# Kernel optimization log

Hardware: AMD Instinct MI355X
Metric: run time of the kernel (lower is better)

## Reference

```python
import jax, jax.numpy as jnp
import numpy as np

DEPTH, HEADS, DIM_HEAD = 3, 8, 64
DIM = 512
MAX_SEQ = 2048
INNER = HEADS * DIM_HEAD  # 512
FF_HID = 4 * DIM          # 2048
EPS = 1e-5


def sparsemax(z):
    # z: (..., n); sparsemax projection onto the simplex (Martins & Astudillo 2016)
    n = z.shape[-1]
    z_sorted = jnp.flip(jnp.sort(z, axis=-1), axis=-1)            # descending
    cs = jnp.cumsum(z_sorted, axis=-1)
    ks = jnp.arange(1, n + 1, dtype=z.dtype)
    support = 1.0 + ks * z_sorted > cs                            # bool
    k_z = jnp.sum(support, axis=-1, keepdims=True)                # int support size
    cs_k = jnp.take_along_axis(cs, k_z - 1, axis=-1)
    tau = (cs_k - 1.0) / k_z.astype(z.dtype)
    return jnp.maximum(z - tau, 0.0)


def layernorm(x, g, b):
    mu = jnp.mean(x, axis=-1, keepdims=True)
    var = jnp.mean(jnp.square(x - mu), axis=-1, keepdims=True)
    return (x - mu) * jax.lax.rsqrt(var + EPS) * g + b


def setup_inputs() -> dict:
    key = jax.random.key(0)
    ks = jax.random.split(key, 12)
    s = 0.02
    inp = {
        "x": jax.random.normal(ks[0], (8, 1024, DIM), dtype=jnp.float32),
        "proj_w": jax.random.normal(ks[1], (DIM, DIM), dtype=jnp.float32) * s,
        "proj_b": jnp.zeros((DIM,), dtype=jnp.float32),
        "pos_emb": jax.random.normal(ks[2], (MAX_SEQ, DIM), dtype=jnp.float32) * s,
        "ln1_g": jnp.ones((DEPTH, DIM), dtype=jnp.float32),
        "ln1_b": jnp.zeros((DEPTH, DIM), dtype=jnp.float32),
        "wqkv": jax.random.normal(ks[3], (DEPTH, DIM, 3 * INNER), dtype=jnp.float32) * s,
        "wout": jax.random.normal(ks[4], (DEPTH, INNER, DIM), dtype=jnp.float32) * s,
        "bout": jnp.zeros((DEPTH, DIM), dtype=jnp.float32),
        "ln2_g": jnp.ones((DEPTH, DIM), dtype=jnp.float32),
        "ln2_b": jnp.zeros((DEPTH, DIM), dtype=jnp.float32),
        "w1": jax.random.normal(ks[5], (DEPTH, DIM, 2 * FF_HID), dtype=jnp.float32) * s,
        "b1": jnp.zeros((DEPTH, 2 * FF_HID), dtype=jnp.float32),
        "w2": jax.random.normal(ks[6], (DEPTH, FF_HID, DIM), dtype=jnp.float32) * s,
        "b2": jnp.zeros((DEPTH, DIM), dtype=jnp.float32),
    }
    return inp


def reference(x, proj_w, proj_b, pos_emb, ln1_g, ln1_b, wqkv, wout, bout,
              ln2_g, ln2_b, w1, b1, w2, b2):
    B, S, D = x.shape
    scale = DIM_HEAD ** -0.5
    x = x @ proj_w + proj_b                       # projection
    x = x + pos_emb[:S][None, :, :]               # positional embedding
    for l in range(DEPTH):
        # --- attention block (Residual(PreNorm(Attention))) ---
        h = layernorm(x, ln1_g[l], ln1_b[l])
        qkv = h @ wqkv[l]                         # (B,S,3*INNER)
        q, k, v = jnp.split(qkv, 3, axis=-1)
        rs = lambda t: t.reshape(B, S, HEADS, DIM_HEAD).transpose(0, 2, 1, 3)
        q, k, v = rs(q), rs(k), rs(v)             # (B,H,S,Dh)
        sim = jnp.einsum('bhid,bhjd->bhij', q, k) * scale
        attn = sparsemax(sim)
        out = jnp.einsum('bhij,bhjd->bhid', attn, v)
        out = out.transpose(0, 2, 1, 3).reshape(B, S, INNER)
        x = x + (out @ wout[l] + bout[l])
        # --- feedforward block (Residual(PreNorm(GEGLU FFN))) ---
        h = layernorm(x, ln2_g[l], ln2_b[l])
        hh = h @ w1[l] + b1[l]                    # (B,S,2*FF_HID)
        a, g = jnp.split(hh, 2, axis=-1)
        ff = (a * jax.nn.gelu(g, approximate=False)) @ w2[l] + b2[l]
        x = x + ff
    return jnp.mean(x, axis=1)                    # (B, D) mean pool
```

## Files before the change

kernel.cpp:

```cpp
#include <hip/hip_runtime.h>
#include <stdint.h>

typedef unsigned short u16;
typedef __attribute__((ext_vector_type(8))) short short8;
typedef __attribute__((ext_vector_type(4))) float f32x4;

__device__ __forceinline__ float bf2f(u16 u){
  union { unsigned u; float f; } v; v.u = ((unsigned)u) << 16; return v.f;
}
__device__ __forceinline__ u16 f2bf(float f){
  union { float f; unsigned u; } v; v.f = f;
  unsigned u = v.u;
  return (u16)((u + 0x7FFFu + ((u >> 16) & 1u)) >> 16);
}
__device__ __forceinline__ void g2lds16(const u16* g, u16* lds){
  __builtin_amdgcn_global_load_lds(
      (const __attribute__((address_space(1))) unsigned int*)g,
      (__attribute__((address_space(3))) unsigned int*)lds, 16, 0, 0);
}

__global__ void k_flag(const unsigned* __restrict__ ln1g, int* __restrict__ flag){
  if (threadIdx.x == 0 && blockIdx.x == 0)
    *flag = (ln1g[0] == 0x3F800000u) ? 0 : 1;
}

__global__ void k_cvt_f32(const void* __restrict__ src, float* __restrict__ dst, int n,
                          const int* __restrict__ flag){
  int i = blockIdx.x * blockDim.x + threadIdx.x;
  if (i < n) dst[i] = (*flag) ? bf2f(((const u16*)src)[i]) : ((const float*)src)[i];
}
__global__ void k_cvt_bf16(const void* __restrict__ src, u16* __restrict__ dst, int n,
                           const int* __restrict__ flag){
  int i = blockIdx.x * blockDim.x + threadIdx.x;
  if (i < n) dst[i] = (*flag) ? ((const u16*)src)[i] : f2bf(((const float*)src)[i]);
}

__global__ void k_transpose(const void* __restrict__ src, u16* __restrict__ dst,
                            int K, int N, const int* __restrict__ flag){
  __shared__ u16 tile[32][33];
  int n0 = blockIdx.x * 32, k0 = blockIdx.y * 32;
  size_t zsrc = (size_t)blockIdx.z * K * N;
  size_t zdst = (size_t)blockIdx.z * N * K;
  int tx = threadIdx.x & 31, ty = threadIdx.x >> 5;
  bool isbf = (*flag) != 0;
  const float* sf = (const float*)src; const u16* sb = (const u16*)src;
  #pragma unroll
  for (int p = 0; p < 4; ++p){
    int kk = k0 + p*8 + ty, nn = n0 + tx;
    size_t idx = zsrc + (size_t)kk * N + nn;
    tile[tx][p*8+ty] = isbf ? sb[idx] : f2bf(sf[idx]);
  }
  __syncthreads();
  #pragma unroll
  for (int p = 0; p < 4; ++p){
    int nn = n0 + p*8 + ty, kk = k0 + tx;
    dst[zdst + (size_t)nn * K + kk] = tile[p*8+ty][tx];
  }
}

__global__ void k_vt(const u16* __restrict__ src, u16* __restrict__ dst){
  __shared__ u16 tile[32][33];
  int d0 = blockIdx.x * 32, s0 = blockIdx.y * 32;
  size_t base = (size_t)blockIdx.z * 65536;
  int tx = threadIdx.x & 31, ty = threadIdx.x >> 5;
  #pragma unroll
  for (int p = 0; p < 4; ++p)
    tile[tx][p*8+ty] = src[base + (size_t)(s0 + p*8 + ty) * 64 + d0 + tx];
  __syncthreads();
  #pragma unroll
  for (int p = 0; p < 4; ++p)
    dst[base + (size_t)(d0 + p*8 + ty) * 1024 + s0 + tx] = tile[p*8+ty][tx];
}

__global__ __launch_bounds__(256) void k_ln(const float* __restrict__ x,
                                            const float* __restrict__ g,
                                            const float* __restrict__ b,
                                            u16* __restrict__ out){
  int row = blockIdx.x, tid = threadIdx.x;
  const float* xr = x + (size_t)row * 512;
  float x0 = xr[tid], x1 = xr[tid + 256];
  float s = x0 + x1, ss = x0*x0 + x1*x1;
  #pragma unroll
  for (int off = 1; off < 64; off <<= 1){ s += __shfl_xor(s, off, 64); ss += __shfl_xor(ss, off, 64); }
  __shared__ float as_[4], bs_[4];
  int wv = tid >> 6, lane = tid & 63;
  if (lane == 0){ as_[wv] = s; bs_[wv] = ss; }
  __syncthreads();
  s = as_[0] + as_[1] + as_[2] + as_[3];
  ss = bs_[0] + bs_[1] + bs_[2] + bs_[3];
  float mu = s * (1.f/512.f);
  float var = ss * (1.f/512.f) - mu*mu;
  float rs = rsqrtf(var + 1e-5f);
  out[(size_t)row*512 + tid]       = f2bf((x0 - mu) * rs * g[tid]       + b[tid]);
  out[(size_t)row*512 + tid + 256] = f2bf((x1 - mu) * rs * g[tid + 256] + b[tid + 256]);
}

__global__ __launch_bounds__(256) void k_gemm(const u16* __restrict__ A,
                                              const u16* __restrict__ Wt, int K, int mode,
                                              float* __restrict__ xres, u16* __restrict__ out16,
                                              const float* __restrict__ bias,
                                              const float* __restrict__ pos){
  __shared__ u16 As[128*64];
  __shared__ u16 Bs[128*64];
  const int tid = threadIdx.x;
  const int wv = tid >> 6, lane = tid & 63;
  const int lm = lane & 15, lq = lane >> 4;
  const int wm = (wv >> 1) * 64, wn = (wv & 1) * 64;
  const int m0 = blockIdx.y * 128, n0 = blockIdx.x * 128;
  const int lrow = lane >> 3;
  const int scol = ((lane & 7) ^ lrow) << 3;
  f32x4 acc[4][4];
  #pragma unroll
  for (int i = 0; i < 4; ++i)
    #pragma unroll
    for (int j = 0; j < 4; ++j){ f32x4 z = {0.f,0.f,0.f,0.f}; acc[i][j] = z; }

  for (int k0 = 0; k0 < K; k0 += 64){
    #pragma unroll
    for (int it = 0; it < 4; ++it){
      int ci = wv*4 + it;
      int row = ci*8 + lrow;
      g2lds16(&A [(size_t)(m0 + row) * K + k0 + scol], &As[ci*512]);
      g2lds16(&Wt[(size_t)(n0 + row) * K + k0 + scol], &Bs[ci*512]);
    }
    __syncthreads();
    #pragma unroll
    for (int kk = 0; kk < 2; ++kk){
      short8 af[4], bf[4];
      #pragma unroll
      for (int t = 0; t < 4; ++t){
        int cs = ((kk*4 + lq) ^ (lm & 7)) << 3;
        af[t] = *(const short8*)&As[(wm + t*16 + lm)*64 + cs];
        bf[t] = *(const short8*)&Bs[(wn + t*16 + lm)*64 + cs];
      }
      #pragma unroll
      for (int i = 0; i < 4; ++i)
        #pragma unroll
        for (int j = 0; j < 4; ++j)
          acc[i][j] = __builtin_amdgcn_mfma_f32_16x16x32_bf16(af[i], bf[j], acc[i][j], 0, 0, 0);
    }
    __syncthreads();
  }
  #pragma unroll
  for (int i = 0; i < 4; ++i)
    #pragma unroll
    for (int j = 0; j < 4; ++j)
      #pragma unroll
      for (int r = 0; r < 4; ++r){
        int row = m0 + wm + i*16 + lq*4 + r;
        int col = n0 + wn + j*16 + lm;
        float v = acc[i][j][r];
        if (mode == 0){
          xres[(size_t)row*512 + col] = v + bias[col] + pos[(size_t)(row & 1023)*512 + col];
        } else if (mode == 1){
          int part = col >> 9, within = col & 511;
          int head = within >> 6, dh = within & 63;
          int b = row >> 10, s = row & 1023;
          out16[(size_t)part*4194304 + (((size_t)(b*8 + head)*1024 + s) << 6) + dh] = f2bf(v);
        } else {
          size_t idx = (size_t)row*512 + col;
          xres[idx] = xres[idx] + v + bias[col];
        }
      }
}

__global__ __launch_bounds__(256) void k_gemm64(const u16* __restrict__ A,
                                                const u16* __restrict__ Wt, int K, int mode,
                                                float* __restrict__ xres,
                                                const float* __restrict__ bias,
                                                const float* __restrict__ pos){
  __shared__ u16 As[64*64];
  __shared__ u16 Bs[128*64];
  const int tid = threadIdx.x;
  const int wv = tid >> 6, lane = tid & 63;
  const int lm = lane & 15, lq = lane >> 4;
  const int wm = (wv >> 1) * 32, wn = (wv & 1) * 64;
  const int m0 = blockIdx.y * 64, n0 = blockIdx.x * 128;
  const int lrow = lane >> 3;
  const int scol = ((lane & 7) ^ lrow) << 3;
  f32x4 acc[2][4];
  #pragma unroll
  for (int i = 0; i < 2; ++i)
    #pragma unroll
    for (int j = 0; j < 4; ++j){ f32x4 z = {0.f,0.f,0.f,0.f}; acc[i][j] = z; }

  for (int k0 = 0; k0 < K; k0 += 64){
    #pragma unroll
    for (int it = 0; it < 2; ++it){
      int ci = wv*2 + it;
      int row = ci*8 + lrow;
      g2lds16(&A[(size_t)(m0 + row) * K + k0 + scol], &As[ci*512]);
    }
    #pragma unroll
    for (int it = 0; it < 4; ++it){
      int ci = wv*4 + it;
      int row = ci*8 + lrow;
      g2lds16(&Wt[(size_t)(n0 + row) * K + k0 + scol], &Bs[ci*512]);
    }
    __syncthreads();
    #pragma unroll
    for (int kk = 0; kk < 2; ++kk){
      short8 af[2], bf[4];
      int cs = ((kk*4 + lq) ^ (lm & 7)) << 3;
      #pragma unroll
      for (int t = 0; t < 2; ++t)
        af[t] = *(const short8*)&As[(wm + t*16 + lm)*64 + cs];
      #pragma unroll
      for (int t = 0; t < 4; ++t)
        bf[t] = *(const short8*)&Bs[(wn + t*16 + lm)*64 + cs];
      #pragma unroll
      for (int i = 0; i < 2; ++i)
        #pragma unroll
        for (int j = 0; j < 4; ++j)
          acc[i][j] = __builtin_amdgcn_mfma_f32_16x16x32_bf16(af[i], bf[j], acc[i][j], 0, 0, 0);
    }
    __syncthreads();
  }
  #pragma unroll
  for (int i = 0; i < 2; ++i)
    #pragma unroll
    for (int j = 0; j < 4; ++j)
      #pragma unroll
      for (int r = 0; r < 4; ++r){
        int row = m0 + wm + i*16 + lq*4 + r;
        int col = n0 + wn + j*16 + lm;
        float v = acc[i][j][r];
        if (mode == 0){
          xres[(size_t)row*512 + col] = v + bias[col] + pos[(size_t)(row & 1023)*512 + col];
        } else {
          size_t idx = (size_t)row*512 + col;
          xres[idx] = xres[idx] + v + bias[col];
        }
      }
}

__global__ __launch_bounds__(256) void k_ff1_geglu64(const u16* __restrict__ A,
                                                     const u16* __restrict__ W1t,
                                                     const float* __restrict__ b1,
                                                     u16* __restrict__ ffh){
  __shared__ u16 As[64*64];
  __shared__ u16 Ba[128*64];
  __shared__ u16 Bg[128*64];
  const int tid = threadIdx.x;
  const int wv = tid >> 6, lane = tid & 63;
  const int lm = lane & 15, lq = lane >> 4;
  const int wm = (wv >> 1) * 32, wn = (wv & 1) * 64;
  const int m0 = blockIdx.y * 64, n0 = blockIdx.x * 128;
  const int lrow = lane >> 3;
  const int scol = ((lane & 7) ^ lrow) << 3;
  const int K = 512;
  f32x4 aa[2][4], ag[2][4];
  #pragma unroll
  for (int i = 0; i < 2; ++i)
    #pragma unroll
    for (int j = 0; j < 4; ++j){ f32x4 z = {0.f,0.f,0.f,0.f}; aa[i][j] = z; ag[i][j] = z; }
  for (int k0 = 0; k0 < K; k0 += 64){
    #pragma unroll
    for (int it = 0; it < 2; ++it){
      int ci = wv*2 + it;
      int row = ci*8 + lrow;
      g2lds16(&A[(size_t)(m0 + row) * K + k0 + scol], &As[ci*512]);
    }
    #pragma unroll
    for (int it = 0; it < 4; ++it){
      int ci = wv*4 + it;
      int row = ci*8 + lrow;
      g2lds16(&W1t[(size_t)(n0 + row) * K + k0 + scol],        &Ba[ci*512]);
      g2lds16(&W1t[(size_t)(2048 + n0 + row) * K + k0 + scol], &Bg[ci*512]);
    }
    __syncthreads();
    #pragma unroll
    for (int kk = 0; kk < 2; ++kk){
      short8 af[2], ba[4], bg[4];
      int cs = ((kk*4 + lq) ^ (lm & 7)) << 3;
      #pragma unroll
      for (int t = 0; t < 2; ++t)
        af[t] = *(const short8*)&As[(wm + t*16 + lm)*64 + cs];
      #pragma unroll
      for (int t = 0; t < 4; ++t){
        ba[t] = *(const short8*)&Ba[(wn + t*16 + lm)*64 + cs];
        bg[t] = *(const short8*)&Bg[(wn + t*16 + lm)*64 + cs];
      }
      #pragma unroll
      for (int i = 0; i < 2; ++i)
        #pragma unroll
        for (int j = 0; j < 4; ++j){
          aa[i][j] = __builtin_amdgcn_mfma_f32_16x16x32_bf16(af[i], ba[j], aa[i][j], 0, 0, 0);
          ag[i][j] = __builtin_amdgcn_mfma_f32_16x16x32_bf16(af[i], bg[j], ag[i][j], 0, 0, 0);
        }
    }
    __syncthreads();
  }
  #pragma unroll
  for (int i = 0; i < 2; ++i)
    #pragma unroll
    for (int j = 0; j < 4; ++j)
      #pragma unroll
      for (int r = 0; r < 4; ++r){
        int row = m0 + wm + i*16 + lq*4 + r;
        int n = n0 + wn + j*16 + lm;
        float a = aa[i][j][r] + b1[n];
        float g = ag[i][j][r] + b1[2048 + n];
        float ge = 0.5f * g * (1.0f + erff(g * 0.70710678118654752440f));
        ffh[(size_t)row*2048 + n] = f2bf(a * ge);
      }
}

__global__ __launch_bounds__(256) void k_qk(const u16* __restrict__ qb,
                                            const u16* __restrict__ kb,
                                            u16* __restrict__ S, int bh0){
  __shared__ u16 As[128*64];
  __shared__ u16 Bs[128*64];
  const int tid = threadIdx.x;
  const int wv = tid >> 6, lane = tid & 63;
  const int lm = lane & 15, lq = lane >> 4;
  const int wm = (wv >> 1) * 64, wn = (wv & 1) * 64;
  const int m0 = blockIdx.y * 128, n0 = blockIdx.x * 128;
  const int lrow = lane >> 3;
  const int scol = ((lane & 7) ^ lrow) << 3;
  const size_t base = (size_t)(bh0 + blockIdx.z) * 65536;
  f32x4 acc[4][4];
  #pragma unroll
  for (int i = 0; i < 4; ++i)
    #pragma unroll
    for (int j = 0; j < 4; ++j){ f32x4 z = {0.f,0.f,0.f,0.f}; acc[i][j] = z; }

  #pragma unroll
  for (int it = 0; it < 4; ++it){
    int ci = wv*4 + it;
    int row = ci*8 + lrow;
    g2lds16(&qb[base + (size_t)(m0 + row) * 64 + scol], &As[ci*512]);
    g2lds16(&kb[base + (size_t)(n0 + row) * 64 + scol], &Bs[ci*512]);
  }
  __syncthreads();
  #pragma unroll
  for (int kk = 0; kk < 2; ++kk){
    short8 af[4], bf[4];
    #pragma unroll
    for (int t = 0; t < 4; ++t){
      int cs = ((kk*4 + lq) ^ (lm & 7)) << 3;
      af[t] = *(const short8*)&As[(wm + t*16 + lm)*64 + cs];
      bf[t] = *(const short8*)&Bs[(wn + t*16 + lm)*64 + cs];
    }
    #pragma unroll
    for (int i = 0; i < 4; ++i)
      #pragma unroll
      for (int j = 0; j < 4; ++j)
        acc[i][j] = __builtin_amdgcn_mfma_f32_16x16x32_bf16(af[i], bf[j], acc[i][j], 0, 0, 0);
  }
  size_t sb = (size_t)blockIdx.z * 1048576;
  #pragma unroll
  for (int i = 0; i < 4; ++i)
    #pragma unroll
    for (int j = 0; j < 4; ++j)
      #pragma unroll
      for (int r = 0; r < 4; ++r){
        int row = m0 + wm + i*16 + lq*4 + r;
        int col = n0 + wn + j*16 + lm;
        S[sb + (size_t)row*1024 + col] = f2bf(acc[i][j][r] * 0.125f);
      }
}

__global__ __launch_bounds__(256) void k_spmax(const u16* __restrict__ S,
                                               u16* __restrict__ P){
  const int lane = threadIdx.x & 63;
  const int row = blockIdx.x * 4 + (threadIdx.x >> 6);
  const u16* src = S + (size_t)row * 1024 + lane * 16;
  u16 zb[16];
  *(uint4*)zb       = *(const uint4*)src;
  *(uint4*)(zb + 8) = *(const uint4*)(src + 8);
  float z[16];
  #pragma unroll
  for (int i = 0; i < 16; ++i) z[i] = bf2f(zb[i]);
  float s = 0.f;
  #pragma unroll
  for (int i = 0; i < 16; ++i) s += z[i];
  #pragma unroll
  for (int off = 1; off < 64; off <<= 1) s += __shfl_xor(s, off, 64);
  float tau = (s - 1.0f) * (1.0f/1024.0f);
  int prevc = 1024;
  for (int it = 0; it < 48; ++it){
    float s2 = 0.f; int c = 0;
    #pragma unroll
    for (int i = 0; i < 16; ++i){
      float p = z[i] - tau;
      s2 += (p > 0.f ? p : 0.f);
      c += (int)__popcll(__ballot(z[i] > tau));
    }
    #pragma unroll
    for (int off = 1; off < 64; off <<= 1) s2 += __shfl_xor(s2, off, 64);
    tau += (s2 - 1.0f) / (float)c;
    if (c == prevc) break;
    prevc = c;
  }
  u16 tmp[16];
  #pragma unroll
  for (int i = 0; i < 16; ++i){
    float p = z[i] - tau; p = p > 0.f ? p : 0.f;
    tmp[i] = f2bf(p);
  }
  u16* dst = P + (size_t)row * 1024 + lane * 16;
  *(uint4*)dst       = *(const uint4*)tmp;
  *(uint4*)(dst + 8) = *(const uint4*)(tmp + 8);
}

__global__ __launch_bounds__(256) void k_pv(const u16* __restrict__ P,
                                            const u16* __restrict__ vt,
                                            u16* __restrict__ aout, int bh0){
  __shared__ u16 As[64*64];
  __shared__ u16 Bs[64*64];
  const int tid = threadIdx.x;
  const int wv = tid >> 6, lane = tid & 63;
  const int lm = lane & 15, lq = lane >> 4;
  const int m0 = blockIdx.x * 64;
  const int bh = bh0 + blockIdx.y;
  const size_t pbase = (size_t)blockIdx.y * 1048576;
  const size_t vbase = (size_t)bh * 65536;
  const int lrow = lane >> 3;
  const int scol = ((lane & 7) ^ lrow) << 3;
  f32x4 acc[4];
  #pragma unroll
  for (int j = 0; j < 4; ++j){ f32x4 z = {0.f,0.f,0.f,0.f}; acc[j] = z; }

  for (int k0 = 0; k0 < 1024; k0 += 64){
    #pragma unroll
    for (int it = 0; it < 2; ++it){
      int ci = wv*2 + it;
      int row = ci*8 + lrow;
      g2lds16(&P [pbase + (size_t)(m0 + row) * 1024 + k0 + scol], &As[ci*512]);
      g2lds16(&vt[vbase + (size_t)row * 1024 + k0 + scol],        &Bs[ci*512]);
    }
    __syncthreads();
    #pragma unroll
    for (int kk = 0; kk < 2; ++kk){
      int csa = ((kk*4 + lq) ^ (lm & 7)) << 3;
      short8 af = *(const short8*)&As[(wv*16 + lm)*64 + csa];
      #pragma unroll
      for (int j = 0; j < 4; ++j){
        short8 bf = *(const short8*)&Bs[(j*16 + lm)*64 + csa];
        acc[j] = __builtin_amdgcn_mfma_f32_16x16x32_bf16(af, bf, acc[j], 0, 0, 0);
      }
    }
    __syncthreads();
  }
  int b = bh >> 3, h = bh & 7;
  #pragma unroll
  for (int j = 0; j < 4; ++j)
    #pragma unroll
    for (int r = 0; r < 4; ++r){
      int s = m0 + wv*16 + lq*4 + r;
      int d = j*16 + lm;
      aout[((size_t)(b*1024 + s))*512 + h*64 + d] = f2bf(acc[j][r]);
    }
}

__global__ __launch_bounds__(256) void k_attn(const u16* __restrict__ qb,
                                              const u16* __restrict__ kb,
                                              const u16* __restrict__ vb,
                                              u16* __restrict__ aout){
  extern __shared__ char smem[];
  float* sc = (float*)smem;
  u16*  P   = (u16*)smem;
  u16*  Qs  = (u16*)(smem + 131072);
  u16*  KVs = (u16*)(smem + 131072 + 4608);
  const int tid = threadIdx.x;
  const int wv = tid >> 6, lane = tid & 63;
  const int lm = lane & 15, lq = lane >> 4;
  const int bh = blockIdx.y, s0 = blockIdx.x * 32;
  const size_t base = (size_t)bh * 65536;
  {
    int r = tid >> 3, c = tid & 7;
    *(uint4*)&Qs[r*72 + (c << 3)] = *(const uint4*)&qb[base + (size_t)(s0 + r)*64 + (c << 3)];
  }
  for (int kt = 0; kt < 16; ++kt){
    __syncthreads();
    #pragma unroll
    for (int it = 0; it < 2; ++it){
      int s = it*256 + tid; int r = s >> 3, c = s & 7;
      *(uint4*)&KVs[r*72 + (c << 3)] =
          *(const uint4*)&kb[base + (size_t)(kt*64 + r)*64 + (c << 3)];
    }
    __syncthreads();
    f32x4 accs[2];
    { f32x4 z = {0.f,0.f,0.f,0.f}; accs[0] = z; accs[1] = z; }
    #pragma unroll
    for (int kk = 0; kk < 2; ++kk){
      short8 bfk = *(const short8*)&KVs[(wv*16 + lm)*72 + kk*32 + lq*8];
      #pragma unroll
      for (int mt = 0; mt < 2; ++mt){
        short8 af = *(const short8*)&Qs[(mt*16 + lm)*72 + kk*32 + lq*8];
        accs[mt] = __builtin_amdgcn_mfma_f32_16x16x32_bf16(af, bfk, accs[mt], 0, 0, 0);
      }
    }
    #pragma unroll
    for (int mt = 0; mt < 2; ++mt)
      #pragma unroll
      for (int r = 0; r < 4; ++r){
        int row = mt*16 + lq*4 + r;
        int col = kt*64 + wv*16 + lm;
        sc[row*1024 + (((col >> 2) ^ (row & 7)) << 2) + (col & 3)] = accs[mt][r] * 0.125f;
      }
  }
  __syncthreads();
  for (int rr = 0; rr < 8; ++rr){
    int row = wv*8 + rr;
    float z[16];
    #pragma unroll
    for (int i = 0; i < 16; ++i){
      int col = lane + (i << 6);
      z[i] = sc[row*1024 + (((col >> 2) ^ (row & 7)) << 2) + (col & 3)];
    }
    bool act[16];
    #pragma unroll
    for (int i = 0; i < 16; ++i) act[i] = true;
    float prevc = -1.f, tau = 0.f;
    for (int it = 0; it < 64; ++it){
      float s = 0.f, c = 0.f;
      #pragma unroll
      for (int i = 0; i < 16; ++i) if (act[i]){ s += z[i]; c += 1.f; }
      #pragma unroll
      for (int off = 1; off < 64; off <<= 1){ s += __shfl_xor(s, off, 64); c += __shfl_xor(c, off, 64); }
      tau = (s - 1.0f) / c;
      if (c == prevc) break;
      prevc = c;
      #pragma unroll
      for (int i = 0; i < 16; ++i) act[i] = z[i] > tau;
    }
    #pragma unroll
    for (int i = 0; i < 16; ++i){
      int col = lane + (i << 6);
      float p = z[i] - tau; p = p > 0.f ? p : 0.f;
      P[row*2048 + (((col >> 3) ^ (row & 7)) << 3) + (col & 7)] = f2bf(p);
    }
  }
  f32x4 acco[2];
  { f32x4 z = {0.f,0.f,0.f,0.f}; acco[0] = z; acco[1] = z; }
  for (int kt = 0; kt < 16; ++kt){
    __syncthreads();
    {
      int dc = tid >> 6, key = tid & 63;
      const u16* src = &vb[base + (size_t)(kt*64 + key)*64 + dc*16];
      u16 tmp[16];
      *(uint4*)tmp       = *(const uint4*)src;
      *(uint4*)(tmp + 8) = *(const uint4*)(src + 8);
      #pragma unroll
      for (int j = 0; j < 16; ++j) KVs[(dc*16 + j)*72 + key] = tmp[j];
    }
    __syncthreads();
    #pragma unroll
    for (int kk = 0; kk < 2; ++kk){
      short8 bfv = *(const short8*)&KVs[(wv*16 + lm)*72 + kk*32 + lq*8];
      #pragma unroll
      for (int mt = 0; mt < 2; ++mt){
        int m = mt*16 + lm;
        int k = kt*64 + kk*32 + lq*8;
        short8 af = *(const short8*)&P[m*2048 + (((k >> 3) ^ (m & 7)) << 3)];
        acco[mt] = __builtin_amdgcn_mfma_f32_16x16x32_bf16(af, bfv, acco[mt], 0, 0, 0);
      }
    }
  }
  int b = bh >> 3, h = bh & 7;
  #pragma unroll
  for (int mt = 0; mt < 2; ++mt)
    #pragma unroll
    for (int r = 0; r < 4; ++r){
      int row = mt*16 + lq*4 + r;
      int s = s0 + row;
      aout[((size_t)(b*1024 + s))*512 + h*64 + wv*16 + lm] = f2bf(acco[mt][r]);
    }
}

__global__ __launch_bounds__(256) void k_pool1(const float* __restrict__ xres,
                                               float* __restrict__ part){
  int b = blockIdx.y, ch = blockIdx.x, tid = threadIdx.x;
  float a0 = 0.f, a1 = 0.f;
  for (int i = 0; i < 64; ++i){
    const float* r = xres + ((size_t)(b*1024 + ch*64 + i)) * 512;
    a0 += r[tid]; a1 += r[tid + 256];
  }
  part[((size_t)(b*16 + ch))*512 + tid]       = a0;
  part[((size_t)(b*16 + ch))*512 + tid + 256] = a1;
}
__global__ __launch_bounds__(512) void k_pool2(const float* __restrict__ part,
                                               void* __restrict__ out,
                                               const int* __restrict__ flag){
  int b = blockIdx.x, d = threadIdx.x;
  float s = 0.f;
  for (int c = 0; c < 16; ++c) s += part[((size_t)(b*16 + c))*512 + d];
  s *= (1.0f/1024.0f);
  if (*flag) ((u16*)out)[b*512 + d] = f2bf(s);
  else       ((float*)out)[b*512 + d] = s;
}

extern "C" void kernel_launch(void* const* d_in, const int* in_sizes, int n_in,
                              void* d_out, int out_size, void* d_ws, size_t ws_size,
                              hipStream_t stream){
  (void)in_sizes; (void)n_in; (void)out_size;
  char* w = (char*)d_ws;
  size_t off = 0;
  auto alloc = [&](size_t bytes) -> char* {
    char* p = w + off;
    off += (bytes + 255) & ~(size_t)255;
    return p;
  };
  int*   flag  = (int*)  alloc(4);
  float* xres  = (float*)alloc((size_t)8192*512*4);
  u16*   hb    = (u16*)  alloc((size_t)8192*512*2);
  u16*   qb    = (u16*)  alloc((size_t)8388608);
  u16*   kb    = (u16*)  alloc((size_t)8388608);
  u16*   vb    = (u16*)  alloc((size_t)8388608);
  u16*   aoutb = (u16*)  alloc((size_t)8388608);
  u16*   ffh   = qb;
  u16*   pwT   = (u16*)  alloc((size_t)512*512*2);
  u16*   wqkvT = (u16*)  alloc((size_t)3*1536*512*2);
  u16*   woutT = (u16*)  alloc((size_t)3*512*512*2);
  u16*   w1T   = (u16*)  alloc((size_t)3*4096*512*2);
  u16*   w2T   = (u16*)  alloc((size_t)3*512*2048*2);
  float* posf  = (float*)alloc((size_t)1024*512*4);
  float* pbf   = (float*)alloc(512*4);
  float* ln1gf = (float*)alloc(1536*4);
  float* ln1bf = (float*)alloc(1536*4);
  float* ln2gf = (float*)alloc(1536*4);
  float* ln2bf = (float*)alloc(1536*4);
  float* boutf = (float*)alloc(1536*4);
  float* b1f   = (float*)alloc(12288*4);
  float* b2f   = (float*)alloc(1536*4);
  float* part  = (float*)alloc((size_t)8*16*512*4);
  u16*   vt    = (u16*)  alloc((size_t)8388608);

  int chunk = 0;
  u16* Sbuf = nullptr; u16* Pbuf = nullptr;
  {
    size_t rem = (ws_size > off) ? (ws_size - off) : 0;
    for (int c = 64; c >= 8; c >>= 1){
      size_t need = (size_t)c * 1048576 * 4 + 512;
      if (need <= rem){
        Sbuf = (u16*)alloc((size_t)c * 1048576 * 2);
        Pbuf = (u16*)alloc((size_t)c * 1048576 * 2);
        chunk = c;
        break;
      }
    }
  }

  const void* x_raw = d_in[0];  const void* projw = d_in[1];  const void* projb = d_in[2];
  const void* pose  = d_in[3];  const void* ln1g  = d_in[4];  const void* ln1b  = d_in[5];
  const void* wqkv  = d_in[6];  const void* wout  = d_in[7];  const void* bout  = d_in[8];
  const void* ln2g  = d_in[9];  const void* ln2b  = d_in[10]; const void* w1    = d_in[11];
  const void* b1    = d_in[12]; const void* w2    = d_in[13]; const void* b2    = d_in[14];

  k_flag<<<1, 1, 0, stream>>>((const unsigned*)ln1g, flag);

  k_transpose<<<dim3(16, 16, 1), 256, 0, stream>>>(projw, pwT,   512,  512, flag);
  k_transpose<<<dim3(48, 16, 3), 256, 0, stream>>>(wqkv,  wqkvT, 512, 1536, flag);
  k_transpose<<<dim3(16, 16, 3), 256, 0, stream>>>(wout,  woutT, 512,  512, flag);
  k_transpose<<<dim3(128,16, 3), 256, 0, stream>>>(w1,    w1T,   512, 4096, flag);
  k_transpose<<<dim3(16, 64, 3), 256, 0, stream>>>(w2,    w2T,  2048,  512, flag);

  k_cvt_f32<<<2,    256, 0, stream>>>(projb, pbf,    512,    flag);
  k_cvt_f32<<<2048, 256, 0, stream>>>(pose,  posf,   524288, flag);
  k_cvt_f32<<<6,    256, 0, stream>>>(ln1g,  ln1gf,  1536,   flag);
  k_cvt_f32<<<6,    256, 0, stream>>>(ln1b,  ln1bf,  1536,   flag);
  k_cvt_f32<<<6,    256, 0, stream>>>(ln2g,  ln2gf,  1536,   flag);
  k_cvt_f32<<<6,    256, 0, stream>>>(ln2b,  ln2bf,  1536,   flag);
  k_cvt_f32<<<6,    256, 0, stream>>>(bout,  boutf,  1536,   flag);
  k_cvt_f32<<<48,   256, 0, stream>>>(b1,    b1f,    12288,  flag);
  k_cvt_f32<<<6,    256, 0, stream>>>(b2,    b2f,    1536,   flag);
  k_cvt_bf16<<<16384, 256, 0, stream>>>(x_raw, hb, 4194304, flag);

  k_gemm64<<<dim3(4, 128), 256, 0, stream>>>(hb, pwT, 512, 0, xres, pbf, posf);

  for (int l = 0; l < 3; ++l){
    k_ln<<<8192, 256, 0, stream>>>(xres, ln1gf + l*512, ln1bf + l*512, hb);
    k_gemm<<<dim3(12, 64), 256, 0, stream>>>(hb, wqkvT + (size_t)l*1536*512, 512, 1,
                                             nullptr, qb, nullptr, nullptr);
    if (chunk){
      k_vt<<<dim3(2, 32, 64), 256, 0, stream>>>(vb, vt);
      for (int bh0 = 0; bh0 < 64; bh0 += chunk){
        k_qk<<<dim3(8, 8, chunk), 256, 0, stream>>>(qb, kb, Sbuf, bh0);
        k_spmax<<<chunk*256, 256, 0, stream>>>(Sbuf, Pbuf);
        k_pv<<<dim3(16, chunk), 256, 0, stream>>>(Pbuf, vt, aoutb, bh0);
      }
    } else {
      k_attn<<<dim3(32, 64), 256, 144896, stream>>>(qb, kb, vb, aoutb);
    }
    k_gemm64<<<dim3(4, 128), 256, 0, stream>>>(aoutb, woutT + (size_t)l*512*512, 512, 2,
                                               xres, boutf + l*512, nullptr);
    k_ln<<<8192, 256, 0, stream>>>(xres, ln2gf + l*512, ln2bf + l*512, hb);
    k_ff1_geglu64<<<dim3(16, 128), 256, 0, stream>>>(hb, w1T + (size_t)l*4096*512,
                                                     b1f + l*4096, ffh);
    k_gemm64<<<dim3(4, 128), 256, 0, stream>>>(ffh, w2T + (size_t)l*512*2048, 2048, 2,
                                               xres, b2f + l*512, nullptr);
  }
  k_pool1<<<dim3(16, 8), 256, 0, stream>>>(xres, part);
  k_pool2<<<8, 512, 0, stream>>>(part, d_out, flag);
}
```

Baseline: 1.113 ms.

## Write V transposed from QKV GEMM, vectorize layernorm, use fast GELU approximation

The QKV GEMM epilogue now writes V directly in the transposed (dh, s) layout, which removes the separate k_vt transpose kernel and its buffer. The fallback attention kernel reads V from that transposed layout. LayerNorm now handles one row per wavefront with vectorized float4 loads and a 16-byte store, so no shared-memory reduction or block sync is needed. The exact erf GELU is replaced with a tanh-style sigmoid approximation, which changes numerics slightly. The transposed V stores in the GEMM epilogue are scattered and may write less efficiently.

```diff
diff --git a/kernel.cpp b/kernel.cpp
--- a/kernel.cpp
+++ b/kernel.cpp
@@ -17,6 +17,10 @@
   __builtin_amdgcn_global_load_lds(
       (const __attribute__((address_space(1))) unsigned int*)g,
       (__attribute__((address_space(3))) unsigned int*)lds, 16, 0, 0);
+}
+__device__ __forceinline__ float gelu_fast(float g){
+  float u2 = g * (1.5957691216057308f + 0.0713548162726f * g * g);
+  return g * __builtin_amdgcn_rcpf(1.0f + __expf(-u2));
 }
 
 __global__ void k_flag(const unsigned* __restrict__ ln1g, int* __restrict__ flag){
@@ -58,41 +62,32 @@
   }
 }
 
-__global__ void k_vt(const u16* __restrict__ src, u16* __restrict__ dst){
-  __shared__ u16 tile[32][33];
-  int d0 = blockIdx.x * 32, s0 = blockIdx.y * 32;
-  size_t base = (size_t)blockIdx.z * 65536;
-  int tx = threadIdx.x & 31, ty = threadIdx.x >> 5;
-  #pragma unroll
-  for (int p = 0; p < 4; ++p)
-    tile[tx][p*8+ty] = src[base + (size_t)(s0 + p*8 + ty) * 64 + d0 + tx];
-  __syncthreads();
-  #pragma unroll
-  for (int p = 0; p < 4; ++p)
-    dst[base + (size_t)(d0 + p*8 + ty) * 1024 + s0 + tx] = tile[p*8+ty][tx];
-}
-
 __global__ __launch_bounds__(256) void k_ln(const float* __restrict__ x,
                                             const float* __restrict__ g,
                                             const float* __restrict__ b,
                                             u16* __restrict__ out){
-  int row = blockIdx.x, tid = threadIdx.x;
-  const float* xr = x + (size_t)row * 512;
-  float x0 = xr[tid], x1 = xr[tid + 256];
-  float s = x0 + x1, ss = x0*x0 + x1*x1;
+  int wv = threadIdx.x >> 6, lane = threadIdx.x & 63;
+  int row = blockIdx.x * 4 + wv;
+  const float* xr = x + (size_t)row * 512 + lane * 8;
+  float4 v0 = *(const float4*)xr;
+  float4 v1 = *(const float4*)(xr + 4);
+  float s  = v0.x+v0.y+v0.z+v0.w + v1.x+v1.y+v1.z+v1.w;
+  float ss = v0.x*v0.x+v0.y*v0.y+v0.z*v0.z+v0.w*v0.w
+           + v1.x*v1.x+v1.y*v1.y+v1.z*v1.z+v1.w*v1.w;
   #pragma unroll
   for (int off = 1; off < 64; off <<= 1){ s += __shfl_xor(s, off, 64); ss += __shfl_xor(ss, off, 64); }
-  __shared__ float as_[4], bs_[4];
-  int wv = tid >> 6, lane = tid & 63;
-  if (lane == 0){ as_[wv] = s; bs_[wv] = ss; }
-  __syncthreads();
-  s = as_[0] + as_[1] + as_[2] + as_[3];
-  ss = bs_[0] + bs_[1] + bs_[2] + bs_[3];
   float mu = s * (1.f/512.f);
   float var = ss * (1.f/512.f) - mu*mu;
   float rs = rsqrtf(var + 1e-5f);
-  out[(size_t)row*512 + tid]       = f2bf((x0 - mu) * rs * g[tid]       + b[tid]);
-  out[(size_t)row*512 + tid + 256] = f2bf((x1 - mu) * rs * g[tid + 256] + b[tid + 256]);
+  const float* gp = g + lane*8; const float* bp = b + lane*8;
+  float4 g0 = *(const float4*)gp, g1 = *(const float4*)(gp+4);
+  float4 b0 = *(const float4*)bp, b1 = *(const float4*)(bp+4);
+  u16 o[8];
+  o[0]=f2bf((v0.x-mu)*rs*g0.x+b0.x); o[1]=f2bf((v0.y-mu)*rs*g0.y+b0.y);
+  o[2]=f2bf((v0.z-mu)*rs*g0.z+b0.z); o[3]=f2bf((v0.w-mu)*rs*g0.w+b0.w);
+  o[4]=f2bf((v1.x-mu)*rs*g1.x+b1.x); o[5]=f2bf((v1.y-mu)*rs*g1.y+b1.y);
+  o[6]=f2bf((v1.z-mu)*rs*g1.z+b1.z); o[7]=f2bf((v1.w-mu)*rs*g1.w+b1.w);
+  *(uint4*)(out + (size_t)row*512 + lane*8) = *(const uint4*)o;
 }
 
 __global__ __launch_bounds__(256) void k_gemm(const u16* __restrict__ A,
@@ -156,7 +151,11 @@
           int part = col >> 9, within = col & 511;
           int head = within >> 6, dh = within & 63;
           int b = row >> 10, s = row & 1023;
-          out16[(size_t)part*4194304 + (((size_t)(b*8 + head)*1024 + s) << 6) + dh] = f2bf(v);
+          int bh = b*8 + head;
+          size_t o;
+          if (part < 2) o = (size_t)part*4194304 + (((size_t)bh*1024 + s) << 6) + dh;
+          else          o = (size_t)8388608 + (size_t)bh*65536 + (size_t)dh*1024 + s;
+          out16[o] = f2bf(v);
         } else {
           size_t idx = (size_t)row*512 + col;
           xres[idx] = xres[idx] + v + bias[col];
@@ -301,8 +300,7 @@
         int n = n0 + wn + j*16 + lm;
         float a = aa[i][j][r] + b1[n];
         float g = ag[i][j][r] + b1[2048 + n];
-        float ge = 0.5f * g * (1.0f + erff(g * 0.70710678118654752440f));
-        ffh[(size_t)row*2048 + n] = f2bf(a * ge);
+        ffh[(size_t)row*2048 + n] = f2bf(a * gelu_fast(g));
       }
 }
 
@@ -456,7 +454,7 @@
 
 __global__ __launch_bounds__(256) void k_attn(const u16* __restrict__ qb,
                                               const u16* __restrict__ kb,
-                                              const u16* __restrict__ vb,
+                                              const u16* __restrict__ vt,
                                               u16* __restrict__ aout){
   extern __shared__ char smem[];
   float* sc = (float*)smem;
@@ -539,12 +537,9 @@
     __syncthreads();
     {
       int dc = tid >> 6, key = tid & 63;
-      const u16* src = &vb[base + (size_t)(kt*64 + key)*64 + dc*16];
-      u16 tmp[16];
-      *(uint4*)tmp       = *(const uint4*)src;
-      *(uint4*)(tmp + 8) = *(const uint4*)(src + 8);
-      #pragma unroll
-      for (int j = 0; j < 16; ++j) KVs[(dc*16 + j)*72 + key] = tmp[j];
+      #pragma unroll
+      for (int j = 0; j < 16; ++j)
+        KVs[(dc*16 + j)*72 + key] = vt[base + (size_t)(dc*16 + j)*1024 + kt*64 + key];
     }
     __syncthreads();
     #pragma unroll
@@ -608,7 +603,7 @@
   u16*   hb    = (u16*)  alloc((size_t)8192*512*2);
   u16*   qb    = (u16*)  alloc((size_t)8388608);
   u16*   kb    = (u16*)  alloc((size_t)8388608);
-  u16*   vb    = (u16*)  alloc((size_t)8388608);
+  u16*   vtb   = (u16*)  alloc((size_t)8388608);
   u16*   aoutb = (u16*)  alloc((size_t)8388608);
   u16*   ffh   = qb;
   u16*   pwT   = (u16*)  alloc((size_t)512*512*2);
@@ -626,7 +621,6 @@
   float* b1f   = (float*)alloc(12288*4);
   float* b2f   = (float*)alloc(1536*4);
   float* part  = (float*)alloc((size_t)8*16*512*4);
-  u16*   vt    = (u16*)  alloc((size_t)8388608);
 
   int chunk = 0;
   u16* Sbuf = nullptr; u16* Pbuf = nullptr;
@@ -671,22 +665,21 @@
   k_gemm64<<<dim3(4, 128), 256, 0, stream>>>(hb, pwT, 512, 0, xres, pbf, posf);
 
   for (int l = 0; l < 3; ++l){
-    k_ln<<<8192, 256, 0, stream>>>(xres, ln1gf + l*512, ln1bf + l*512, hb);
+    k_ln<<<2048, 256, 0, stream>>>(xres, ln1gf + l*512, ln1bf + l*512, hb);
     k_gemm<<<dim3(12, 64), 256, 0, stream>>>(hb, wqkvT + (size_t)l*1536*512, 512, 1,
                                              nullptr, qb, nullptr, nullptr);
     if (chunk){
-      k_vt<<<dim3(2, 32, 64), 256, 0, stream>>>(vb, vt);
       for (int bh0 = 0; bh0 < 64; bh0 += chunk){
         k_qk<<<dim3(8, 8, chunk), 256, 0, stream>>>(qb, kb, Sbuf, bh0);
         k_spmax<<<chunk*256, 256, 0, stream>>>(Sbuf, Pbuf);
-        k_pv<<<dim3(16, chunk), 256, 0, stream>>>(Pbuf, vt, aoutb, bh0);
+        k_pv<<<dim3(16, chunk), 256, 0, stream>>>(Pbuf, vtb, aoutb, bh0);
       }
     } else {
-      k_attn<<<dim3(32, 64), 256, 144896, stream>>>(qb, kb, vb, aoutb);
+      k_attn<<<dim3(32, 64), 256, 144896, stream>>>(qb, kb, vtb, aoutb);
     }
     k_gemm64<<<dim3(4, 128), 256, 0, stream>>>(aoutb, woutT + (size_t)l*512*512, 512, 2,
                                                xres, boutf + l*512, nullptr);
-    k_ln<<<8192, 256, 0, stream>>>(xres, ln2gf + l*512, ln2bf + l*512, hb);
+    k_ln<<<2048, 256, 0, stream>>>(xres, ln2gf + l*512, ln2bf + l*512, hb);
     k_ff1_geglu64<<<dim3(16, 128), 256, 0, stream>>>(hb, w1T + (size_t)l*4096*512,
                                                      b1f + l*4096, ffh);
     k_gemm64<<<dim3(4, 128), 256, 0, stream>>>(ffh, w2T + (size_t)l*512*2048, 2048, 2,
```

New measurement: 1.041 ms. 1.07x faster.
